# Kernel tuning notes

Measured on AMD Instinct MI355X. Metric: run time of the kernel, lower is better.

## Reference

```python
import jax, jax.numpy as jnp
import numpy as np

TEMPERATURE = 0.5  # init kwarg: temperature
EPS = 1e-8         # torch CosineSimilarity eps


def setup_inputs() -> dict:
    key = jax.random.key(0)
    k1, k2 = jax.random.split(key)
    B, D = 2048, 256
    return {
        "z_i": jax.random.normal(k1, (B, D), dtype=jnp.float32),
        "z_j": jax.random.normal(k2, (B, D), dtype=jnp.float32),
    }


def reference(z_i, z_j):
    # NT-Xent (SimCLR) loss, world_size = 1.
    B = z_i.shape[0]
    N = 2 * B
    z = jnp.concatenate([z_i, z_j], axis=0)                       # [N, D]
    # Cosine similarity = normalized dot product (fused normalize + matmul,
    # avoiding the torch broadcast NxNxD intermediate).
    zn = z / jnp.clip(jnp.linalg.norm(z, axis=1, keepdims=True), EPS)
    sim = (zn @ zn.T) / TEMPERATURE                               # [N, N]
    # Positive pair similarity for each row: diag offsets +B and -B.
    pos = jnp.concatenate([jnp.diagonal(sim, offset=B),
                           jnp.diagonal(sim, offset=-B)], axis=0)  # [N]
    # CrossEntropy with label 0 over logits [pos, negatives] equals
    # -pos + logsumexp over {pos} U negatives = all off-diagonal entries,
    # since the mask removes exactly the diagonal and the positive pair
    # (which is re-added as `pos`). Mask diagonal with -inf.
    neg_inf = jnp.finfo(sim.dtype).min
    sim_masked = jnp.where(jnp.eye(N, dtype=bool), neg_inf, sim)
    lse = jax.scipy.special.logsumexp(sim_masked, axis=1)          # [N]
    # reduction='sum' then / N  ->  mean over rows
    loss = jnp.sum(lse - pos) / N
    return loss
```

## Files before the change

kernel.cpp:

```cpp
#include <hip/hip_runtime.h>


#define NROWS 4096
#define DDIM 256
#define BHALF 2048
#define TILE 128
#define BK 64
#define LDP 72
#define NCB 32
#define INV_T 2.0f

typedef short bf16x8 __attribute__((ext_vector_type(8)));
typedef float f32x4 __attribute__((ext_vector_type(4)));

__device__ inline unsigned short f2bf(float f) {
    union { float f; unsigned u; } c; c.f = f;
    unsigned u = c.u + 0x7fffu + ((c.u >> 16) & 1u);
    return (unsigned short)(u >> 16);
}

__global__ __launch_bounds__(256) void k_normalize(
    const float* __restrict__ zi, const float* __restrict__ zj,
    unsigned short* __restrict__ zn, float* __restrict__ out) {
    if (blockIdx.x == 0 && threadIdx.x == 0) out[0] = 0.f;
    const int wave = threadIdx.x >> 6, lane = threadIdx.x & 63;
    const int row = blockIdx.x * 4 + wave;
    const float* src = (row < BHALF) ? (zi + row * DDIM)
                                     : (zj + (row - BHALF) * DDIM);
    const float4 v = ((const float4*)src)[lane];
    float ss = v.x * v.x + v.y * v.y + v.z * v.z + v.w * v.w;
    #pragma unroll
    for (int m = 1; m < 64; m <<= 1) ss += __shfl_xor(ss, m);
    const float scale = 1.0f / fmaxf(sqrtf(ss), 1e-8f);
    ushort4 o;
    o.x = f2bf(v.x * scale); o.y = f2bf(v.y * scale);
    o.z = f2bf(v.z * scale); o.w = f2bf(v.w * scale);
    ((ushort4*)(zn + row * DDIM))[lane] = o;
}

__global__ __launch_bounds__(256) void k_simlse(
    const unsigned short* __restrict__ zn,
    float* __restrict__ partial,
    float* __restrict__ posv) {
    __shared__ unsigned short As[TILE * LDP];
    __shared__ unsigned short Bs[TILE * LDP];
    __shared__ float pscratch[TILE];
    __shared__ float cscratch[TILE];

    int t = blockIdx.x, bx = 0, rem = NCB;
    while (t >= rem) { t -= rem; ++bx; --rem; }
    const int by = bx + t;

    const int tid = threadIdx.x;
    const int wave = tid >> 6, lane = tid & 63;
    const int quad = lane >> 4, l15 = lane & 15;
    const int wr = wave >> 1, wc = wave & 1;
    const int rowBase = bx * TILE;
    const int colBase = by * TILE;

    f32x4 acc[4][4] = {};

    #pragma unroll
    for (int kb = 0; kb < DDIM / BK; ++kb) {
        __syncthreads();
        #pragma unroll
        for (int i = 0; i < 4; ++i) {
            const int flat = tid + i * 256;
            const int r = flat >> 3, c = flat & 7;
            *(bf16x8*)&As[r * LDP + c * 8] =
                *(const bf16x8*)&zn[(rowBase + r) * DDIM + kb * BK + c * 8];
            *(bf16x8*)&Bs[r * LDP + c * 8] =
                *(const bf16x8*)&zn[(colBase + r) * DDIM + kb * BK + c * 8];
        }
        __syncthreads();
        #pragma unroll
        for (int s = 0; s < 2; ++s) {
            bf16x8 af[4], bf[4];
            #pragma unroll
            for (int mt = 0; mt < 4; ++mt)
                af[mt] = *(const bf16x8*)&As[(wr * 64 + mt * 16 + l15) * LDP + s * 32 + quad * 8];
            #pragma unroll
            for (int nt = 0; nt < 4; ++nt)
                bf[nt] = *(const bf16x8*)&Bs[(wc * 64 + nt * 16 + l15) * LDP + s * 32 + quad * 8];
            #pragma unroll
            for (int mt = 0; mt < 4; ++mt)
                #pragma unroll
                for (int nt = 0; nt < 4; ++nt)
                    acc[mt][nt] = __builtin_amdgcn_mfma_f32_16x16x32_bf16(
                        af[mt], bf[nt], acc[mt][nt], 0, 0, 0);
        }
    }

    float rsum[4][4];
    float csum[4] = {};
    #pragma unroll
    for (int mt = 0; mt < 4; ++mt) {
        #pragma unroll
        for (int r = 0; r < 4; ++r) {
            const int grow = rowBase + wr * 64 + mt * 16 + quad * 4 + r;
            float s = 0.f;
            #pragma unroll
            for (int nt = 0; nt < 4; ++nt) {
                const int gcol = colBase + wc * 64 + nt * 16 + l15;
                const float simv = acc[mt][nt][r] * INV_T;
                const float e = (gcol != grow) ? __expf(simv) : 0.f;
                s += e;
                csum[nt] += e;
                if (gcol == grow + BHALF) {
                    posv[grow] = simv;
                    posv[gcol] = simv;
                }
            }
            s += __shfl_xor(s, 1); s += __shfl_xor(s, 2);
            s += __shfl_xor(s, 4); s += __shfl_xor(s, 8);
            rsum[mt][r] = s;
        }
    }
    #pragma unroll
    for (int nt = 0; nt < 4; ++nt) {
        csum[nt] += __shfl_xor(csum[nt], 16);
        csum[nt] += __shfl_xor(csum[nt], 32);
    }

    __syncthreads();
    if (wc == 0 && l15 == 0) {
        #pragma unroll
        for (int mt = 0; mt < 4; ++mt)
            #pragma unroll
            for (int r = 0; r < 4; ++r)
                pscratch[wr * 64 + mt * 16 + quad * 4 + r] = rsum[mt][r];
    }
    if (wr == 0 && quad == 0) {
        #pragma unroll
        for (int nt = 0; nt < 4; ++nt)
            cscratch[wc * 64 + nt * 16 + l15] = csum[nt];
    }
    __syncthreads();
    if (wc == 1 && l15 == 0) {
        #pragma unroll
        for (int mt = 0; mt < 4; ++mt)
            #pragma unroll
            for (int r = 0; r < 4; ++r) {
                const int lr = wr * 64 + mt * 16 + quad * 4 + r;
                partial[by * NROWS + rowBase + lr] = rsum[mt][r] + pscratch[lr];
            }
    }
    if (bx != by && wr == 1 && quad == 0) {
        #pragma unroll
        for (int nt = 0; nt < 4; ++nt) {
            const int lc = wc * 64 + nt * 16 + l15;
            partial[bx * NROWS + colBase + lc] = csum[nt] + cscratch[lc];
        }
    }
}

__global__ __launch_bounds__(256) void k_rowlse(
    const float* __restrict__ partial, const float* __restrict__ posv,
    float* __restrict__ out) {
    __shared__ float red[4];
    const int tid = threadIdx.x;
    const int row = blockIdx.x * 256 + tid;
    float s = 0.f;
    #pragma unroll
    for (int p = 0; p < NCB; ++p) s += partial[p * NROWS + row];
    float v = __logf(s) - posv[row];
    #pragma unroll
    for (int m = 1; m < 64; m <<= 1) v += __shfl_xor(v, m);
    if ((tid & 63) == 0) red[tid >> 6] = v;
    __syncthreads();
    if (tid == 0)
        atomicAdd(out, (red[0] + red[1] + red[2] + red[3]) * (1.0f / (float)NROWS));
}

extern "C" void kernel_launch(void* const* d_in, const int* in_sizes, int n_in,
                              void* d_out, int out_size, void* d_ws, size_t ws_size,
                              hipStream_t stream) {
    const float* zi = (const float*)d_in[0];
    const float* zj = (const float*)d_in[1];
    float* out = (float*)d_out;

    unsigned short* zn = (unsigned short*)d_ws;
    float* partial = (float*)((char*)d_ws + NROWS * DDIM * 2);
    float* posv = partial + NCB * NROWS;

    k_normalize<<<NROWS / 4, 256, 0, stream>>>(zi, zj, zn, out);
    k_simlse<<<NCB * (NCB + 1) / 2, 256, 0, stream>>>(zn, partial, posv);
    k_rowlse<<<16, 256, 0, stream>>>(partial, posv, out);
}
```

Measured before the change: 78.15 us.

## Fuse row LSE reduction into sim kernel via atomics and last-block finalize

Replaces the per-column-block partial buffer with atomic accumulation into a per-row sum, and removes the third kernel launch by having the last finishing block, detected through a global atomic counter, compute the log-sum-exp minus positive term and write the loss. Normalization now also zeroes the row sums and the counter. This saves one launch and the partial-buffer traffic, but adds atomic contention on row sums and makes the floating-point summation order nondeterministic.

```diff
diff --git a/kernel.cpp b/kernel.cpp
--- a/kernel.cpp
+++ b/kernel.cpp
@@ -8,6 +8,7 @@
 #define BK 64
 #define LDP 72
 #define NCB 32
+#define NBLK 528
 #define INV_T 2.0f
 
 typedef short bf16x8 __attribute__((ext_vector_type(8)));
@@ -21,8 +22,10 @@
 
 __global__ __launch_bounds__(256) void k_normalize(
     const float* __restrict__ zi, const float* __restrict__ zj,
-    unsigned short* __restrict__ zn, float* __restrict__ out) {
-    if (blockIdx.x == 0 && threadIdx.x == 0) out[0] = 0.f;
+    unsigned short* __restrict__ zn, float* __restrict__ rowsum,
+    unsigned* __restrict__ counter, float* __restrict__ out) {
+    if (blockIdx.x == 0 && threadIdx.x == 0) { *counter = 0u; out[0] = 0.f; }
+    if (threadIdx.x < 4) rowsum[blockIdx.x * 4 + threadIdx.x] = 0.f;
     const int wave = threadIdx.x >> 6, lane = threadIdx.x & 63;
     const int row = blockIdx.x * 4 + wave;
     const float* src = (row < BHALF) ? (zi + row * DDIM)
@@ -40,12 +43,15 @@
 
 __global__ __launch_bounds__(256) void k_simlse(
     const unsigned short* __restrict__ zn,
-    float* __restrict__ partial,
-    float* __restrict__ posv) {
+    float* __restrict__ rowsum,
+    float* __restrict__ posv,
+    unsigned* __restrict__ counter,
+    float* __restrict__ out) {
     __shared__ unsigned short As[TILE * LDP];
     __shared__ unsigned short Bs[TILE * LDP];
     __shared__ float pscratch[TILE];
     __shared__ float cscratch[TILE];
+    __shared__ unsigned lastFlag;
 
     int t = blockIdx.x, bx = 0, rem = NCB;
     while (t >= rem) { t -= rem; ++bx; --rem; }
@@ -107,8 +113,10 @@
                 s += e;
                 csum[nt] += e;
                 if (gcol == grow + BHALF) {
-                    posv[grow] = simv;
-                    posv[gcol] = simv;
+                    __hip_atomic_store(&posv[grow], simv, __ATOMIC_RELAXED,
+                                       __HIP_MEMORY_SCOPE_AGENT);
+                    __hip_atomic_store(&posv[gcol], simv, __ATOMIC_RELAXED,
+                                       __HIP_MEMORY_SCOPE_AGENT);
                 }
             }
             s += __shfl_xor(s, 1); s += __shfl_xor(s, 2);
@@ -142,34 +150,45 @@
             #pragma unroll
             for (int r = 0; r < 4; ++r) {
                 const int lr = wr * 64 + mt * 16 + quad * 4 + r;
-                partial[by * NROWS + rowBase + lr] = rsum[mt][r] + pscratch[lr];
+                atomicAdd(&rowsum[rowBase + lr], rsum[mt][r] + pscratch[lr]);
             }
     }
     if (bx != by && wr == 1 && quad == 0) {
         #pragma unroll
         for (int nt = 0; nt < 4; ++nt) {
             const int lc = wc * 64 + nt * 16 + l15;
-            partial[bx * NROWS + colBase + lc] = csum[nt] + cscratch[lc];
-        }
-    }
-}
-
-__global__ __launch_bounds__(256) void k_rowlse(
-    const float* __restrict__ partial, const float* __restrict__ posv,
-    float* __restrict__ out) {
-    __shared__ float red[4];
-    const int tid = threadIdx.x;
-    const int row = blockIdx.x * 256 + tid;
-    float s = 0.f;
-    #pragma unroll
-    for (int p = 0; p < NCB; ++p) s += partial[p * NROWS + row];
-    float v = __logf(s) - posv[row];
-    #pragma unroll
-    for (int m = 1; m < 64; m <<= 1) v += __shfl_xor(v, m);
-    if ((tid & 63) == 0) red[tid >> 6] = v;
-    __syncthreads();
-    if (tid == 0)
-        atomicAdd(out, (red[0] + red[1] + red[2] + red[3]) * (1.0f / (float)NROWS));
+            atomicAdd(&rowsum[colBase + lc], csum[nt] + cscratch[lc]);
+        }
+    }
+
+    __syncthreads();
+    if (tid == 0) {
+        __threadfence();
+        unsigned old = __hip_atomic_fetch_add(counter, 1u, __ATOMIC_ACQ_REL,
+                                              __HIP_MEMORY_SCOPE_AGENT);
+        lastFlag = (old == NBLK - 1) ? 1u : 0u;
+    }
+    __syncthreads();
+    if (lastFlag) {
+        __threadfence();
+        float accv = 0.f;
+        #pragma unroll
+        for (int i = 0; i < NROWS / 256; ++i) {
+            const int row = tid + i * 256;
+            const float s = __hip_atomic_load(&rowsum[row], __ATOMIC_RELAXED,
+                                              __HIP_MEMORY_SCOPE_AGENT);
+            const float pv = __hip_atomic_load(&posv[row], __ATOMIC_RELAXED,
+                                               __HIP_MEMORY_SCOPE_AGENT);
+            accv += __logf(s) - pv;
+        }
+        #pragma unroll
+        for (int m = 1; m < 64; m <<= 1) accv += __shfl_xor(accv, m);
+        if ((tid & 63) == 0) pscratch[tid >> 6] = accv;
+        __syncthreads();
+        if (tid == 0)
+            out[0] = (pscratch[0] + pscratch[1] + pscratch[2] + pscratch[3])
+                     * (1.0f / (float)NROWS);
+    }
 }
 
 extern "C" void kernel_launch(void* const* d_in, const int* in_sizes, int n_in,
@@ -180,10 +199,10 @@
     float* out = (float*)d_out;
 
     unsigned short* zn = (unsigned short*)d_ws;
-    float* partial = (float*)((char*)d_ws + NROWS * DDIM * 2);
-    float* posv = partial + NCB * NROWS;
-
-    k_normalize<<<NROWS / 4, 256, 0, stream>>>(zi, zj, zn, out);
-    k_simlse<<<NCB * (NCB + 1) / 2, 256, 0, stream>>>(zn, partial, posv);
-    k_rowlse<<<16, 256, 0, stream>>>(partial, posv, out);
-}
+    float* posv = (float*)((char*)d_ws + NROWS * DDIM * 2);
+    float* rowsum = posv + NROWS;
+    unsigned* counter = (unsigned*)(rowsum + NROWS);
+
+    k_normalize<<<NROWS / 4, 256, 0, stream>>>(zi, zj, zn, rowsum, counter, out);
+    k_simlse<<<NBLK, 256, 0, stream>>>(zn, rowsum, posv, counter, out);
+}
```

Result: slower. 90.47 us (+15.8%).
